# Performance work log

Hardware: AMD Instinct MI355X
Metric: run time of the kernel (lower is better)

## Reference

```python
import jax, jax.numpy as jnp
import numpy as np

H = 2048        # hidden_size
NH = 16         # num query heads
NKV = 4         # num kv heads
HD = H // NH    # head_dim = 128
G = NH // NKV   # kv groups = 4
EPS = 1e-12


def setup_inputs() -> dict:
    key = jax.random.key(0)
    ks = jax.random.split(key, 20)
    B, S = 2, 2048
    s = 1.0 / np.sqrt(H)
    inp = {
        "hidden_states": jax.random.normal(ks[0], (B, S, H), jnp.float32),
        "source_states": jax.random.normal(ks[1], (B, S, H), jnp.float32),
        # weights stored [in, out] so y = x @ W + b
        "Wq": jax.random.normal(ks[2], (H, NH * HD), jnp.float32) * s,
        "bq": jnp.zeros((NH * HD,), jnp.float32),
        "Wk": jax.random.normal(ks[3], (H, NKV * HD), jnp.float32) * s,
        "bk": jnp.zeros((NKV * HD,), jnp.float32),
        "Wv": jax.random.normal(ks[4], (H, NKV * HD), jnp.float32) * s,
        "bv": jnp.zeros((NKV * HD,), jnp.float32),
        "Wd": jax.random.normal(ks[5], (H, H), jnp.float32) * s,
        "bd": jnp.zeros((H,), jnp.float32),
        "W1": jax.random.normal(ks[6], (H, H), jnp.float32) * s,
        "b1": jnp.zeros((H,), jnp.float32),
        "W2": jax.random.normal(ks[7], (H, H), jnp.float32) * s,
        "b2": jnp.zeros((H,), jnp.float32),
        "gamma": jnp.ones((H,), jnp.float32),
        "beta": jnp.zeros((H,), jnp.float32),
    }
    return inp


def _layernorm(x, gamma, beta):
    mu = jnp.mean(x, axis=-1, keepdims=True)
    var = jnp.mean(jnp.square(x - mu), axis=-1, keepdims=True)
    return (x - mu) * jax.lax.rsqrt(var + EPS) * gamma + beta


def reference(hidden_states, source_states, Wq, bq, Wk, bk, Wv, bv, Wd, bd,
              W1, b1, W2, b2, gamma, beta):
    B, Sq, _ = hidden_states.shape
    Ss = source_states.shape[1]
    # FFN-gate on source: Pl1 = relu(lin1(src)); P = lin2(Pl1) + Pl1
    Pl1 = jax.nn.relu(source_states @ W1 + b1)
    P = (Pl1 @ W2 + b2) + Pl1
    # projections; K/V grouped into NKV heads, Q into NH = NKV*G heads
    K = (P @ Wk + bk).reshape(B, Ss, NKV, HD).transpose(0, 2, 1, 3)        # b k s d
    V = (P @ Wv + bv).reshape(B, Ss, NKV, HD).transpose(0, 2, 1, 3)        # b k s d
    Q = (hidden_states @ Wq + bq).reshape(B, Sq, NKV, G, HD)
    Q = Q.transpose(0, 2, 3, 1, 4)                                          # b k g q d
    scores = jnp.einsum('bkgqd,bksd->bkgqs', Q, K) / np.sqrt(HD)
    probs = jax.nn.softmax(scores, axis=-1)
    ctx = jnp.einsum('bkgqs,bksd->bkgqd', probs, V)                         # b k g q d
    ctx = ctx.transpose(0, 3, 1, 2, 4).reshape(B, Sq, NH * HD)              # b q h*d
    out = ctx @ Wd + bd
    return _layernorm(out + hidden_states, gamma, beta)
```

## Files before the change

kernel.cpp:

```cpp
#include <hip/hip_runtime.h>
#include <hip/hip_bf16.h>

typedef __bf16 bf16;
typedef __bf16 bf16x2 __attribute__((ext_vector_type(2)));
typedef __bf16 bf16x4 __attribute__((ext_vector_type(4)));
typedef __bf16 bf16x8 __attribute__((ext_vector_type(8)));
typedef float  f32x4  __attribute__((ext_vector_type(4)));
typedef unsigned int u32x4 __attribute__((ext_vector_type(4)));

#define H_   2048
#define S_   2048
#define B_   2
#define NH_  16
#define NKV_ 4
#define HD_  128
#define KVS  1024

#define QSCALE 0.12751743f

__device__ __forceinline__ f32x4 mfma16(bf16x8 a, bf16x8 b, f32x4 c) {
  return __builtin_amdgcn_mfma_f32_16x16x32_bf16(a, b, c, 0, 0, 0);
}

typedef __attribute__((address_space(3))) unsigned int lds_u32_t;
typedef const __attribute__((address_space(1))) unsigned int glb_u32_t;
__device__ __forceinline__ void glds16(const bf16* g, bf16* l) {
  __builtin_amdgcn_global_load_lds((glb_u32_t*)g, (lds_u32_t*)l, 16, 0, 0);
}

__device__ __forceinline__ unsigned pk2(float a, float b) {
  bf16x2 v = { (bf16)a, (bf16)b };
  return __builtin_bit_cast(unsigned, v);
}


__global__ __launch_bounds__(256)
void prep(const float* __restrict__ Wq, const float* __restrict__ W1,
          const float* __restrict__ W2, const float* __restrict__ Wd,
          const float* __restrict__ Wk, const float* __restrict__ Wv,
          const float* __restrict__ hidden, const float* __restrict__ source,
          bf16* __restrict__ Wqt, bf16* __restrict__ W1t,
          bf16* __restrict__ W2t, bf16* __restrict__ Wdt,
          bf16* __restrict__ Wkt, bf16* __restrict__ Wvt,
          bf16* __restrict__ hb,  bf16* __restrict__ sb)
{
  __shared__ bf16 t[32][33];
  int idx = blockIdx.x;
  if (idx < 16384) {
    const float* in = (idx < 8192) ? hidden : source;
    bf16*       out = (idx < 8192) ? hb : sb;
    const int i = idx & 8191;
    const size_t off = ((size_t)i * 256 + threadIdx.x) * 4;
    const float4 v = *(const float4*)(in + off);
    bf16x4 o = { (bf16)v.x, (bf16)v.y, (bf16)v.z, (bf16)v.w };
    *(bf16x4*)(out + off) = o;
    return;
  }
  idx -= 16384;
  const float* in; bf16* out; int N;
  if      (idx < 4096)  { in = Wq; out = Wqt; N = 2048; }
  else if (idx < 8192)  { in = W1; out = W1t; N = 2048; idx -= 4096; }
  else if (idx < 12288) { in = W2; out = W2t; N = 2048; idx -= 8192; }
  else if (idx < 16384) { in = Wd; out = Wdt; N = 2048; idx -= 12288; }
  else if (idx < 17408) { in = Wk; out = Wkt; N = 512;  idx -= 16384; }
  else                  { in = Wv; out = Wvt; N = 512;  idx -= 17408; }
  const int K = 2048;
  const int tx = threadIdx.x & 31, ty = threadIdx.x >> 5;
  const int k0 = (idx & 63) * 32, n0 = (idx >> 6) * 32;
  #pragma unroll
  for (int i = 0; i < 4; i++)
    t[ty + i*8][tx] = (bf16)in[(size_t)(k0 + ty + i*8) * N + n0 + tx];
  __syncthreads();
  #pragma unroll
  for (int i = 0; i < 4; i++)
    out[(size_t)(n0 + ty + i*8) * K + k0 + tx] = t[tx][ty + i*8];
}

__device__ __forceinline__
void gemm_body(const bf16* __restrict__ A, const bf16* __restrict__ Wt,
               const float* __restrict__ bias, const float* __restrict__ bias2,
               int nsplit, const bf16* __restrict__ resid,
               bf16* __restrict__ outB, bf16* __restrict__ outC,
               int N, int K, int relu, float oscale, int mode,
               int m0, int n0, bf16* As, bf16* Bs)
{
  const int tid  = threadIdx.x;
  const int lane = tid & 63;
  const int w    = tid >> 6;
  const int wm = w & 1, wn = w >> 1;
  const int quad = lane >> 4, l16 = lane & 15;
  const int g_r = lane >> 2;
  const int g_c = (lane & 3) * 8;

  const f32x4 fz = {0.f, 0.f, 0.f, 0.f};
  f32x4 acc[4][4];
  #pragma unroll
  for (int i = 0; i < 4; i++)
    #pragma unroll
    for (int j = 0; j < 4; j++) acc[i][j] = fz;

  auto stage = [&](int nb, int k0) {
    #pragma unroll
    for (int i = 0; i < 2; i++) {
      const int rb = (w*2 + i) * 16;
      glds16(A  + (size_t)(m0 + rb + g_r) * K + k0 + g_c, As + nb*4096 + rb*32 + lane*8);
      glds16(Wt + (size_t)(n0 + rb + g_r) * K + k0 + g_c, Bs + nb*4096 + rb*32 + lane*8);
    }
  };

  stage(0, 0);
  const int NK = K >> 5;
  for (int it = 0; it < NK; it++) {
    const int bf = it & 1;
    __syncthreads();
    if (it + 1 < NK) stage(bf ^ 1, (it + 1) << 5);
    bf16x8 af[4], bfr[4];
    #pragma unroll
    for (int i = 0; i < 4; i++)
      af[i]  = *(const bf16x8*)(As + bf*4096 + (wm*64 + i*16 + l16)*32 + quad*8);
    #pragma unroll
    for (int j = 0; j < 4; j++)
      bfr[j] = *(const bf16x8*)(Bs + bf*4096 + (wn*64 + j*16 + l16)*32 + quad*8);
    #pragma unroll
    for (int i = 0; i < 4; i++)
      #pragma unroll
      for (int j = 0; j < 4; j++)
        acc[i][j] = mfma16(af[i], bfr[j], acc[i][j]);
  }

  #pragma unroll
  for (int i = 0; i < 4; i++) {
    const int row = m0 + wm*64 + i*16 + quad*4;
    #pragma unroll
    for (int j = 0; j < 4; j++) {
      const int col = n0 + wn*64 + j*16 + l16;
      const float bi = (col < nsplit) ? bias[col] : bias2[col - nsplit];
      #pragma unroll
      for (int r = 0; r < 4; r++) {
        float v = acc[i][j][r] + bi;
        if (relu) v = fmaxf(v, 0.f);
        v *= oscale;
        const int rowg = row + r;
        if (mode == 0) {
          size_t idx = (size_t)rowg * N + col;
          if (resid) v += (float)resid[idx];
          outB[idx] = (bf16)v;
        } else if (mode == 1) {
          const int bb = rowg >> 11, s = rowg & 2047;
          if (col < 512) {
            const int kvq = col >> 7, d = col & 127;
            size_t off = ((size_t)((bb*4 + kvq)*64 + (s >> 5))) * 4096
                       + ((d >> 5)*2 + ((s >> 4) & 1)) * 512
                       + (((d >> 3) & 3)*16 + (s & 15)) * 8 + (d & 7);
            outB[off] = (bf16)v;
          } else {
            const int kvq = (col - 512) >> 7, d = (col - 512) & 127;
            size_t off = ((size_t)((bb*4 + kvq)*64 + (s >> 5))) * 4096
                       + (d >> 4) * 512
                       + (((s & 31) >> 3)*16 + (d & 15)) * 8 + (s & 7);
            outC[off] = (bf16)v;
          }
        } else {
          const int bb = rowg >> 11, q = rowg & 2047;
          const int hh = col >> 7, d = col & 127;
          size_t off = ((size_t)((bb*16 + hh)*64 + (q >> 5))) * 4096
                     + ((d >> 5)*2 + ((q >> 4) & 1)) * 512
                     + (((d >> 3) & 3)*16 + (q & 15)) * 8 + (d & 7);
          outB[off] = (bf16)v;
        }
      }
    }
  }
}

__global__ __launch_bounds__(256)
void gemm_one(const bf16* __restrict__ A, const bf16* __restrict__ Wt,
              const float* __restrict__ bias, const float* __restrict__ bias2,
              int nsplit, const bf16* __restrict__ resid,
              bf16* __restrict__ outB, bf16* __restrict__ outC,
              int N, int K, int relu, float oscale, int mode)
{
  __shared__ __align__(16) bf16 As[2*128*32];
  __shared__ __align__(16) bf16 Bs[2*128*32];
  gemm_body(A, Wt, bias, bias2, nsplit, resid, outB, outC, N, K, relu, oscale,
            mode, blockIdx.y*128, blockIdx.x*128, As, Bs);
}

__global__ __launch_bounds__(256)
void gemm_dual(const bf16* __restrict__ A0, const bf16* __restrict__ W0,
               const float* __restrict__ b0, bf16* __restrict__ o0,
               int relu0, float s0,
               const bf16* __restrict__ A1, const bf16* __restrict__ W1,
               const float* __restrict__ b1, bf16* __restrict__ o1,
               int relu1, float s1, int N, int K)
{
  __shared__ __align__(16) bf16 As[2*128*32];
  __shared__ __align__(16) bf16 Bs[2*128*32];
  if (blockIdx.z == 0)
    gemm_body(A0, W0, b0, b0, 1<<30, nullptr, o0, nullptr, N, K, relu0, s0,
              2 , blockIdx.y*128, blockIdx.x*128, As, Bs);
  else
    gemm_body(A1, W1, b1, b1, 1<<30, nullptr, o1, nullptr, N, K, relu1, s1,
              0, blockIdx.y*128, blockIdx.x*128, As, Bs);
}

__global__ __launch_bounds__(256)
void attn_partial(const bf16* __restrict__ QF, const bf16* __restrict__ KF,
                  const bf16* __restrict__ VF, bf16* __restrict__ OpBase,
                  float* __restrict__ LsBase)
{
  __shared__ __align__(16) bf16 Ks[3*4096];
  __shared__ __align__(16) bf16 Vs[3*4096];
  const int tid = threadIdx.x;
  const int lane = tid & 63, w = tid >> 6;
  const int quad = lane >> 4, l16 = lane & 15;
  const int qt = blockIdx.x, h = blockIdx.y;
  const int b = blockIdx.z >> 1, sh = blockIdx.z & 1;
  const int kv = h >> 2;
  const int qbase = qt * 128 + w * 32;

  bf16*  Op = OpBase + (size_t)sh * 8388608;
  float* Lp = LsBase + (size_t)sh * (B_*NH_*S_);

  const bf16* Ktile = KF + ((size_t)((b*4 + kv) * 64)) * 4096;
  const bf16* Vtile = VF + ((size_t)((b*4 + kv) * 64)) * 4096;
  const bf16* Qt    = QF + ((size_t)((b*16 + h) * 64 + (qbase >> 5))) * 4096;

  const f32x4 fz = {0.f, 0.f, 0.f, 0.f};

  bf16x8 qf[2][4];
  #pragma unroll
  for (int i = 0; i < 2; i++)
    #pragma unroll
    for (int kt = 0; kt < 4; kt++)
      qf[i][kt] = *(const bf16x8*)(Qt + (kt*2 + i)*512 + lane*8);

  f32x4 o[2][8];
  #pragma unroll
  for (int i = 0; i < 2; i++)
    #pragma unroll
    for (int n = 0; n < 8; n++) o[i][n] = fz;
  float lsum[2] = {0.f, 0.f};

  auto stageKV = [&](int nb, int t5) {
    const bf16* kt_ = Ktile + (size_t)t5 * 4096;
    const bf16* vt_ = Vtile + (size_t)t5 * 4096;
    bf16* Kb = Ks + nb*4096;
    bf16* Vb = Vs + nb*4096;
    glds16(kt_ + (w*2+0)*512 + lane*8, Kb + (w*2+0)*512 + lane*8);
    glds16(kt_ + (w*2+1)*512 + lane*8, Kb + (w*2+1)*512 + lane*8);
    glds16(vt_ + (w    )*512 + lane*8, Vb + (w    )*512 + lane*8);
    glds16(vt_ + (4+w  )*512 + lane*8, Vb + (4+w  )*512 + lane*8);
  };

  const int t5b = sh * 32;
  stageKV(0, t5b);
  stageKV(1, t5b + 1);

  const int NIT = 32;
  int cur = 0;
  for (int it = 0; it < NIT; it++) {
    if (it < NIT - 1) { asm volatile("s_waitcnt vmcnt(4)" ::: "memory"); }
    else              { asm volatile("s_waitcnt vmcnt(0)" ::: "memory"); }
    __builtin_amdgcn_sched_barrier(0);
    __builtin_amdgcn_s_barrier();
    __builtin_amdgcn_sched_barrier(0);
    if (it + 2 < NIT) {
      int pre = cur + 2; if (pre >= 3) pre -= 3;
      stageKV(pre, t5b + it + 2);
    }

    const bf16* Kb = Ks + cur*4096;
    const bf16* Vb = Vs + cur*4096;
    f32x4 sa[2][2];
    sa[0][0] = fz; sa[0][1] = fz; sa[1][0] = fz; sa[1][1] = fz;
    __builtin_amdgcn_s_setprio(1);
    #pragma unroll
    for (int kt = 0; kt < 4; kt++) {
      bf16x8 kf0 = *(const bf16x8*)(Kb + (kt*2+0)*512 + lane*8);
      bf16x8 kf1 = *(const bf16x8*)(Kb + (kt*2+1)*512 + lane*8);
      #pragma unroll
      for (int i = 0; i < 2; i++) {
        sa[i][0] = mfma16(kf0, qf[i][kt], sa[i][0]);
        sa[i][1] = mfma16(kf1, qf[i][kt], sa[i][1]);
      }
    }
    __builtin_amdgcn_s_setprio(0);

    bf16x8 pf[2];
    #pragma unroll
    for (int i = 0; i < 2; i++) {
      float p[2][4];
      #pragma unroll
      for (int nt = 0; nt < 2; nt++)
        #pragma unroll
        for (int r = 0; r < 4; r++) {
          p[nt][r] = exp2f(sa[i][nt][r]);
          lsum[i] += p[nt][r];
        }
      unsigned Apk = pk2(p[0][0], p[0][1]);
      unsigned Bpk = pk2(p[0][2], p[0][3]);
      unsigned Cpk = pk2(p[1][0], p[1][1]);
      unsigned Dpk = pk2(p[1][2], p[1][3]);
      const int srcL = l16 + ((quad & 1) << 5);
      const bool hi = (quad >= 2);
      const unsigned a0 = __shfl(Apk, srcL),      b0 = __shfl(Bpk, srcL);
      const unsigned a1 = __shfl(Apk, srcL + 16), b1 = __shfl(Bpk, srcL + 16);
      const unsigned c0 = __shfl(Cpk, srcL),      d0 = __shfl(Dpk, srcL);
      const unsigned c1 = __shfl(Cpk, srcL + 16), d1 = __shfl(Dpk, srcL + 16);
      u32x4 t;
      t.x = hi ? c0 : a0;
      t.y = hi ? d0 : b0;
      t.z = hi ? c1 : a1;
      t.w = hi ? d1 : b1;
      pf[i] = __builtin_bit_cast(bf16x8, t);
    }

    __builtin_amdgcn_s_setprio(1);
    #pragma unroll
    for (int nt = 0; nt < 8; nt++) {
      bf16x8 vf = *(const bf16x8*)(Vb + nt*512 + lane*8);
      o[0][nt] = mfma16(pf[0], vf, o[0][nt]);
      o[1][nt] = mfma16(pf[1], vf, o[1][nt]);
    }
    __builtin_amdgcn_s_setprio(0);

    cur = (cur == 2) ? 0 : cur + 1;
  }

  bf16* op = Op + ((size_t)b * S_ + qbase) * H_ + h * HD_;
  #pragma unroll
  for (int i = 0; i < 2; i++)
    #pragma unroll
    for (int nt = 0; nt < 8; nt++)
      #pragma unroll
      for (int r = 0; r < 4; r++)
        op[(size_t)(i*16 + quad*4 + r) * H_ + nt*16 + l16] = (bf16)o[i][nt][r];

  float* lp = Lp + (size_t)(b * NH_ + h) * S_ + qbase;
  #pragma unroll
  for (int i = 0; i < 2; i++) {
    float s = lsum[i];
    s += __shfl_xor(s, 16);
    s += __shfl_xor(s, 32);
    if (lane < 16) lp[i*16 + lane] = s;
  }
}

__global__ __launch_bounds__(256)
void attn_combine(const bf16* __restrict__ O0, const bf16* __restrict__ O1,
                  const float* __restrict__ L0, const float* __restrict__ L1,
                  bf16* __restrict__ ctx)
{
  const int row = blockIdx.x;
  const int b = row >> 11, s = row & 2047;
  const int tid = threadIdx.x;
  const int h = tid >> 4;
  const size_t idx = (size_t)row * H_ + tid * 8;
  const size_t li  = (size_t)(b * NH_ + h) * S_ + s;
  const float rinv = 1.f / (L0[li] + L1[li]);
  bf16x8 a = *(const bf16x8*)(O0 + idx);
  bf16x8 c = *(const bf16x8*)(O1 + idx);
  bf16x8 o;
  #pragma unroll
  for (int k = 0; k < 8; k++)
    o[k] = (bf16)(((float)a[k] + (float)c[k]) * rinv);
  *(bf16x8*)(ctx + idx) = o;
}

__global__ __launch_bounds__(256)
void ln_fused(const bf16* __restrict__ a, const float* __restrict__ hidden,
              const float* __restrict__ gamma, const float* __restrict__ beta,
              float* __restrict__ out)
{
  __shared__ float red[8];
  const int row = blockIdx.x;
  const bf16*  pa = a      + (size_t)row * H_;
  const float* pb = hidden + (size_t)row * H_;
  float x[8]; float s = 0.f, s2 = 0.f;
  #pragma unroll
  for (int j = 0; j < 8; j++) {
    int c = threadIdx.x + j*256;
    float v = (float)pa[c] + pb[c];
    x[j] = v; s += v; s2 += v*v;
  }
  #pragma unroll
  for (int off = 1; off < 64; off <<= 1) {
    s  += __shfl_xor(s,  off);
    s2 += __shfl_xor(s2, off);
  }
  const int wv = threadIdx.x >> 6;
  if ((threadIdx.x & 63) == 0) { red[wv] = s; red[4 + wv] = s2; }
  __syncthreads();
  s  = red[0] + red[1] + red[2] + red[3];
  s2 = red[4] + red[5] + red[6] + red[7];
  const float mu   = s * (1.0f / H_);
  const float var  = s2 * (1.0f / H_) - mu * mu;
  const float rstd = rsqrtf(var + 1e-12f);
  float* po = out + (size_t)row * H_;
  #pragma unroll
  for (int j = 0; j < 8; j++) {
    int c = threadIdx.x + j*256;
    po[c] = ((x[j] - mu) * rstd) * gamma[c] + beta[c];
  }
}

extern "C" void kernel_launch(void* const* d_in, const int* in_sizes, int n_in,
                              void* d_out, int out_size, void* d_ws, size_t ws_size,
                              hipStream_t stream)
{
  (void)in_sizes; (void)n_in; (void)out_size; (void)ws_size;
  const float* hidden = (const float*)d_in[0];
  const float* source = (const float*)d_in[1];
  const float* Wq = (const float*)d_in[2];
  const float* bq = (const float*)d_in[3];
  const float* Wk = (const float*)d_in[4];
  const float* bk = (const float*)d_in[5];
  const float* Wv = (const float*)d_in[6];
  const float* bv = (const float*)d_in[7];
  const float* Wd = (const float*)d_in[8];
  const float* bd = (const float*)d_in[9];
  const float* W1 = (const float*)d_in[10];
  const float* b1 = (const float*)d_in[11];
  const float* W2 = (const float*)d_in[12];
  const float* b2 = (const float*)d_in[13];
  const float* gamma = (const float*)d_in[14];
  const float* beta  = (const float*)d_in[15];

  char* ws = (char*)d_ws;
  const size_t M = 1048576;
  bf16*  rHB = (bf16*)(ws + 0*M);
  bf16*  rSB = (bf16*)(ws + 16*M);
  bf16*  QF  = (bf16*)(ws + 32*M);
  bf16*  Wqt = (bf16*)(ws + 48*M);
  bf16*  W2t = (bf16*)(ws + 56*M);
  bf16*  W1t = (bf16*)(ws + 64*M);
  bf16*  Wdt = (bf16*)(ws + 72*M);
  bf16*  Wkt = (bf16*)(ws + 80*M);
  bf16*  Wvt = (bf16*)(ws + 82*M);
  bf16*  Pl1 = (bf16*)(ws + 84*M);
  bf16*  KF  = (bf16*)(ws + 84*M);
  bf16*  VF  = (bf16*)(ws + 88*M);
  float* Ls  = (float*)(ws + 48*M);
  bf16*  Pb  = rHB;
  bf16*  O0  = rHB;
  bf16*  ctx = (bf16*)(ws + 56*M);
  bf16*  oFb = QF;

  prep<<<34816, 256, 0, stream>>>(Wq, W1, W2, Wd, Wk, Wv, hidden, source,
                                  Wqt, W1t, W2t, Wdt, Wkt, Wvt, rHB, rSB);
  gemm_dual<<<dim3(16,32,2), 256, 0, stream>>>(
      rHB, Wqt, bq, QF,  0, QSCALE,
      rSB, W1t, b1, Pl1, 1, 1.0f, 2048, 2048);
  gemm_one<<<dim3(16,32), 256, 0, stream>>>(Pl1, W2t, b2, b2, 1<<30, Pl1,
                                            Pb, nullptr, 2048, 2048, 0, 1.0f, 0);
  gemm_one<<<dim3(8,32), 256, 0, stream>>>(Pb, Wkt, bk, bv, 512, nullptr,
                                           KF, VF, 1024, 2048, 0, 1.0f, 1);
  attn_partial<<<dim3(16,16,4), 256, 0, stream>>>(QF, KF, VF, O0, Ls);
  attn_combine<<<4096, 256, 0, stream>>>(O0, rSB, Ls, Ls + B_*NH_*S_, ctx);
  gemm_one<<<dim3(16,32), 256, 0, stream>>>(ctx, Wdt, bd, bd, 1<<30, nullptr,
                                            oFb, nullptr, 2048, 2048, 0, 1.0f, 0);
  ln_fused<<<4096, 256, 0, stream>>>(oFb, hidden, gamma, beta, (float*)d_out);
}
```

Baseline: 597.4 us.

## Triple-buffer GEMM LDS pipeline and swizzle workgroups across XCDs

The GEMM mainloop moves from a double buffer to a triple buffer that prefetches two k-tiles ahead. Each iteration waits on vmcnt for the oldest stage and uses a raw s_barrier, so the global-to-LDS copies overlap more with the MFMA work. The GEMM and attention kernels also remap block indices with an XCD-aware swizzle, so neighbouring tiles run on the same XCD and can share its L2. The cost is 50% more LDS per block, which may lower occupancy, and the hardcoded vmcnt count depends on how many loads each stage issues.

```diff
diff --git a/kernel.cpp b/kernel.cpp
--- a/kernel.cpp
+++ b/kernel.cpp
@@ -31,6 +31,12 @@
 __device__ __forceinline__ unsigned pk2(float a, float b) {
   bf16x2 v = { (bf16)a, (bf16)b };
   return __builtin_bit_cast(unsigned, v);
+}
+
+__device__ __forceinline__ int xcd_swz(int orig, int nwg) {
+  const int q = nwg >> 3, r = nwg & 7;
+  const int xcd = orig & 7, off = orig >> 3;
+  return (xcd < r ? xcd * (q + 1) : r * (q + 1) + (xcd - r) * q) + off;
 }
 
 
@@ -109,23 +115,32 @@
   };
 
   stage(0, 0);
+  stage(1, 32);
   const int NK = K >> 5;
+  int cur = 0;
   for (int it = 0; it < NK; it++) {
-    const int bf = it & 1;
-    __syncthreads();
-    if (it + 1 < NK) stage(bf ^ 1, (it + 1) << 5);
+    if (it < NK - 1) { asm volatile("s_waitcnt vmcnt(4)" ::: "memory"); }
+    else             { asm volatile("s_waitcnt vmcnt(0)" ::: "memory"); }
+    __builtin_amdgcn_sched_barrier(0);
+    __builtin_amdgcn_s_barrier();
+    __builtin_amdgcn_sched_barrier(0);
+    if (it + 2 < NK) {
+      int pre = cur + 2; if (pre >= 3) pre -= 3;
+      stage(pre, (it + 2) << 5);
+    }
     bf16x8 af[4], bfr[4];
     #pragma unroll
     for (int i = 0; i < 4; i++)
-      af[i]  = *(const bf16x8*)(As + bf*4096 + (wm*64 + i*16 + l16)*32 + quad*8);
+      af[i]  = *(const bf16x8*)(As + cur*4096 + (wm*64 + i*16 + l16)*32 + quad*8);
     #pragma unroll
     for (int j = 0; j < 4; j++)
-      bfr[j] = *(const bf16x8*)(Bs + bf*4096 + (wn*64 + j*16 + l16)*32 + quad*8);
+      bfr[j] = *(const bf16x8*)(Bs + cur*4096 + (wn*64 + j*16 + l16)*32 + quad*8);
     #pragma unroll
     for (int i = 0; i < 4; i++)
       #pragma unroll
       for (int j = 0; j < 4; j++)
         acc[i][j] = mfma16(af[i], bfr[j], acc[i][j]);
+    cur = (cur == 2) ? 0 : cur + 1;
   }
 
   #pragma unroll
@@ -180,10 +195,13 @@
               bf16* __restrict__ outB, bf16* __restrict__ outC,
               int N, int K, int relu, float oscale, int mode)
 {
-  __shared__ __align__(16) bf16 As[2*128*32];
-  __shared__ __align__(16) bf16 Bs[2*128*32];
+  __shared__ __align__(16) bf16 As[3*4096];
+  __shared__ __align__(16) bf16 Bs[3*4096];
+  const int nwg = gridDim.x * gridDim.y;
+  const int wg = xcd_swz(blockIdx.y * gridDim.x + blockIdx.x, nwg);
+  const int bx = wg % gridDim.x, by = wg / gridDim.x;
   gemm_body(A, Wt, bias, bias2, nsplit, resid, outB, outC, N, K, relu, oscale,
-            mode, blockIdx.y*128, blockIdx.x*128, As, Bs);
+            mode, by*128, bx*128, As, Bs);
 }
 
 __global__ __launch_bounds__(256)
@@ -194,14 +212,17 @@
                const float* __restrict__ b1, bf16* __restrict__ o1,
                int relu1, float s1, int N, int K)
 {
-  __shared__ __align__(16) bf16 As[2*128*32];
-  __shared__ __align__(16) bf16 Bs[2*128*32];
+  __shared__ __align__(16) bf16 As[3*4096];
+  __shared__ __align__(16) bf16 Bs[3*4096];
+  const int nwg = gridDim.x * gridDim.y;
+  const int wg = xcd_swz(blockIdx.y * gridDim.x + blockIdx.x, nwg);
+  const int bx = wg % gridDim.x, by = wg / gridDim.x;
   if (blockIdx.z == 0)
     gemm_body(A0, W0, b0, b0, 1<<30, nullptr, o0, nullptr, N, K, relu0, s0,
-              2 , blockIdx.y*128, blockIdx.x*128, As, Bs);
+              2 , by*128, bx*128, As, Bs);
   else
     gemm_body(A1, W1, b1, b1, 1<<30, nullptr, o1, nullptr, N, K, relu1, s1,
-              0, blockIdx.y*128, blockIdx.x*128, As, Bs);
+              0, by*128, bx*128, As, Bs);
 }
 
 __global__ __launch_bounds__(256)
@@ -214,8 +235,10 @@
   const int tid = threadIdx.x;
   const int lane = tid & 63, w = tid >> 6;
   const int quad = lane >> 4, l16 = lane & 15;
-  const int qt = blockIdx.x, h = blockIdx.y;
-  const int b = blockIdx.z >> 1, sh = blockIdx.z & 1;
+  const int wg = xcd_swz(((int)blockIdx.z * 16 + (int)blockIdx.y) * 16 + (int)blockIdx.x, 1024);
+  const int qt = wg & 15, h = (wg >> 4) & 15;
+  const int bz = wg >> 8;
+  const int b = bz >> 1, sh = bz & 1;
   const int kv = h >> 2;
   const int qbase = qt * 128 + w * 32;
 
```

Result: no change. 585.9 us (-1.9%).
